# Kernel tuning notes

Hardware: AMD Instinct MI355X
Metric: run time of the kernel (lower is better)

The kernel has to match this reference:

```python
import jax, jax.numpy as jnp
import numpy as np

DIM = 768

def setup_inputs() -> dict:
    key = jax.random.key(0)
    k1, k2, k3, k4, k5 = jax.random.split(key, 5)
    B, S, D = 16, 1024, DIM
    x = jax.random.normal(k1, (B, S, D), dtype=jnp.float32)
    # torch Linear weights: W has shape [out, in], y = x @ W.T + b
    w_qkv = jax.random.normal(k2, (3 * D, D), dtype=jnp.float32) * (D ** -0.5)
    b_qkv = jax.random.normal(k3, (3 * D,), dtype=jnp.float32) * 0.01
    w_out = jax.random.normal(k4, (D, D), dtype=jnp.float32) * (D ** -0.5)
    b_out = jax.random.normal(k5, (D,), dtype=jnp.float32) * 0.01
    return {"x": x, "w_qkv": w_qkv, "b_qkv": b_qkv, "w_out": w_out, "b_out": b_out}

def reference(x, w_qkv, b_qkv, w_out, b_out):
    D = x.shape[-1]
    qkv = jnp.einsum('bsd,ed->bse', x, w_qkv) + b_qkv  # [B,S,3D]
    q, k, v = jnp.split(qkv, 3, axis=-1)
    scale = D ** -0.5
    att = jnp.einsum('bqd,bkd->bqk', q, k) * scale  # [B,S,S]
    att = jax.nn.softmax(att, axis=-1)
    # dropout (p=0.1) is identity in eval mode
    out = jnp.einsum('bqk,bkd->bqd', att, v)
    return jnp.einsum('bsd,ed->bse', out, w_out) + b_out
```

## Files before the change

kernel.cpp:

```cpp
#include <hip/hip_runtime.h>
#include <hip/hip_bf16.h>
#include <math.h>

typedef __attribute__((ext_vector_type(8))) short bf16x8;
typedef __attribute__((ext_vector_type(4))) float f32x4;

__device__ __forceinline__ unsigned short f2bf_rne(float f) {
    union { float f; unsigned u; } x; x.f = f;
    unsigned r = x.u + 0x7FFFu + ((x.u >> 16) & 1u);
    return (unsigned short)(r >> 16);
}
__device__ __forceinline__ float bf2f(unsigned short u) {
    union { unsigned u; float f; } x; x.u = ((unsigned)u) << 16; return x.f;
}

__device__ __forceinline__ void store4(unsigned short* p, float v0, float v1, float v2, float v3) {
    ushort4 o; o.x = f2bf_rne(v0); o.y = f2bf_rne(v1); o.z = f2bf_rne(v2); o.w = f2bf_rne(v3);
    *(ushort4*)p = o;
}
__device__ __forceinline__ void store4(float* p, float v0, float v1, float v2, float v3) {
    float4 o; o.x = v0; o.y = v1; o.z = v2; o.w = v3;
    *(float4*)p = o;
}

__device__ __forceinline__ void async_copy16(const void* g, void* l) {
    __builtin_amdgcn_global_load_lds(
        (const __attribute__((address_space(1))) void*)g,
        (__attribute__((address_space(3))) void*)l, 16, 0, 0);
}

__global__ __launch_bounds__(256) void cvt_all(
    const float* __restrict__ x, const float* __restrict__ wo,
    unsigned short* __restrict__ xb, unsigned short* __restrict__ wob,
    float4* __restrict__ z1, float4* __restrict__ z2,
    int n4x, int n4o, int n4r, int n4z)
{
    int j = blockIdx.x * 256 + threadIdx.x;
    const float* in; unsigned short* out;
    if (j < n4x) { in = x; out = xb; }
    else {
        j -= n4x;
        if (j < n4o) { in = wo; out = wob; }
        else {
            j -= n4o;
            if (j < n4r) { float4 z = {0.f, 0.f, 0.f, 0.f}; z1[j] = z; return; }
            j -= n4r;
            if (j < n4z) { float4 z = {0.f, 0.f, 0.f, 0.f}; z2[j] = z; }
            return;
        }
    }
    float4 v = ((const float4*)in)[j];
    ushort4 o;
    o.x = f2bf_rne(v.x); o.y = f2bf_rne(v.y);
    o.z = f2bf_rne(v.z); o.w = f2bf_rne(v.w);
    ((ushort4*)out)[j] = o;
}

__global__ __launch_bounds__(256) void prep(
    const float* __restrict__ w_qkv, const float* __restrict__ b_qkv,
    const float* __restrict__ w_out, const float* __restrict__ b_out,
    unsigned short* __restrict__ wqT, unsigned short* __restrict__ wkT,
    unsigned short* __restrict__ wvT,
    float* __restrict__ v1f, float* __restrict__ v2f,
    float* __restrict__ bpp, float* __restrict__ cbuf)
{
    const int blk = blockIdx.x;
    const int t   = threadIdx.x;
    if (blk < 432) {
        __shared__ float sh[64][65];
        __shared__ float pv[4][64];
        const int m  = blk / 144;
        const int r  = blk % 144;
        const int ty = r / 12;
        const int tx = r % 12;
        const float* W = w_qkv + (long long)m * 768 * 768;
        unsigned short* WT = (m == 0) ? wqT : (m == 1) ? wkT : wvT;
        const float* bsrc = (m == 0) ? (b_qkv + 768) : b_qkv;
        const int il = t & 63;
        const int ob = t >> 6;
        float acc = 0.f;
#pragma unroll
        for (int it = 0; it < 16; ++it) {
            const int ol = ob + it * 4;
            float w = W[(long long)(ty * 64 + ol) * 768 + tx * 64 + il];
            sh[ol][il] = w;
            if (m < 2) acc += w * bsrc[ty * 64 + ol];
        }
        __syncthreads();
#pragma unroll
        for (int it = 0; it < 16; ++it) {
            const int il2 = ob + it * 4;
            WT[(long long)(tx * 64 + il2) * 768 + ty * 64 + il] = f2bf_rne(sh[il][il2]);
        }
        if (m < 2) {
            pv[ob][il] = acc;
            __syncthreads();
            if (t < 64) {
                float s = pv[0][t] + pv[1][t] + pv[2][t] + pv[3][t];
                atomicAdd((m == 0 ? v1f : v2f) + tx * 64 + t, s);
            }
        }
    } else if (blk < 624) {
        const int d = (blk - 432) * 4 + (t >> 6);
        const int l = t & 63;
        float s = 0.f;
        for (int o = l; o < 768; o += 64)
            s += w_out[(long long)d * 768 + o] * b_qkv[1536 + o];
        for (int off = 1; off < 64; off <<= 1) s += __shfl_xor(s, off);
        if (l == 0) bpp[d] = b_out[d] + s;
    } else {
        if (t < 64) {
            float s = 0.f;
            for (int o = t; o < 768; o += 64) s += b_qkv[o] * b_qkv[768 + o];
            for (int off = 1; off < 64; off <<= 1) s += __shfl_xor(s, off);
            if (t == 0) cbuf[0] = s;
        }
    }
}

__global__ __launch_bounds__(256) void finishprep(
    const float* __restrict__ v1f, const float* __restrict__ v2f,
    unsigned short* __restrict__ B2)
{
    int i = blockIdx.x * 256 + threadIdx.x;
    if (i < 768) {
        B2[1536LL * 768 + i] = f2bf_rne(v1f[i]);
        B2[1537LL * 768 + i] = f2bf_rne(v2f[i]);
    }
}

template <typename OutT, bool DO_EXP, bool DO_RSCALE, bool DO_VT>
__global__ __launch_bounds__(256) void gemm_nt_bf16(
    const unsigned short* __restrict__ A, int lda, long long strideA,
    const unsigned short* __restrict__ B, int ldb, long long strideB,
    OutT* __restrict__ C, int ldc, long long strideC,
    const float* __restrict__ bias, float scale, int K,
    float* __restrict__ rowsum, const float* __restrict__ rscale,
    unsigned short* __restrict__ vtp)
{
    __shared__ unsigned short shA[128 * 64];
    __shared__ unsigned short shB[128 * 64];

    const int t    = threadIdx.x;
    const int lane = t & 63;
    const int wave = t >> 6;
    const int wm   = (wave & 1) * 64;
    const int wn   = (wave >> 1) * 64;
    const int quad = lane >> 4;
    const int l16  = lane & 15;

    const int gx = gridDim.x, gy = gridDim.y;
    const int nwg = gx * gy * gridDim.z;
    const int orig = blockIdx.x + gx * (blockIdx.y + gy * blockIdx.z);
    const int id  = (orig & 7) * (nwg >> 3) + (orig >> 3);
    const int bx  = id % gx;
    const int rem = id / gx;
    const int by  = rem % gy;
    const int bz  = rem / gy;

    const long long batch = bz;
    A += batch * strideA;
    B += batch * strideB;
    C += batch * strideC;

    const long long tileM = (long long)by * 128;
    const long long tileN = (long long)bx * 128;
    const long long rowsPerBatch = (long long)gy * 128;

    f32x4 acc[4][4];
#pragma unroll
    for (int i = 0; i < 4; ++i)
#pragma unroll
        for (int j = 0; j < 4; ++j)
#pragma unroll
            for (int r = 0; r < 4; ++r) acc[i][j][r] = 0.0f;

    for (int k0 = 0; k0 < K; k0 += 64) {
        __syncthreads();
#pragma unroll
        for (int p = 0; p < 4; ++p) {
            const int g   = p * 256 + t;
            const int row = g >> 3;
            const int kg  = (g & 7) ^ (row & 7);
            async_copy16(A + (tileM + row) * (long long)lda + k0 + kg * 8, &shA[g << 3]);
            async_copy16(B + (tileN + row) * (long long)ldb + k0 + kg * 8, &shB[g << 3]);
        }
        __syncthreads();

#pragma unroll 1
        for (int h = 0; h < 2; ++h) {
            bf16x8 af[4], bfr[4];
#pragma unroll
            for (int mi = 0; mi < 4; ++mi) {
                const int row = wm + mi * 16 + l16;
                const int kg  = ((h << 2) | quad) ^ (row & 7);
                af[mi] = *(const bf16x8*)(&shA[row * 64 + kg * 8]);
            }
#pragma unroll
            for (int ni = 0; ni < 4; ++ni) {
                const int row = wn + ni * 16 + l16;
                const int kg  = ((h << 2) | quad) ^ (row & 7);
                bfr[ni] = *(const bf16x8*)(&shB[row * 64 + kg * 8]);
            }
#pragma unroll
            for (int mi = 0; mi < 4; ++mi)
#pragma unroll
                for (int ni = 0; ni < 4; ++ni)
                    acc[mi][ni] = __builtin_amdgcn_mfma_f32_16x16x32_bf16(
                        bfr[ni], af[mi], acc[mi][ni], 0, 0, 0);
        }
    }

    const bool vt_block = DO_VT && (tileN >= 768) && (tileN < 1536);
    float cadd = 0.f;
    if (DO_EXP) cadd = rscale[0];
#pragma unroll
    for (int mi = 0; mi < 4; ++mi) {
        const long long gm = tileM + wm + mi * 16 + l16;
        float w = scale;
        if (DO_RSCALE) w = scale / rscale[batch * rowsPerBatch + gm];
        float uq = 0.f;
        if (DO_EXP) uq = bf2f(A[gm * (long long)lda + K + 768]) + cadd;
        float rsum = 0.0f;
#pragma unroll
        for (int ni = 0; ni < 4; ++ni) {
            const long long gn0 = tileN + wn + ni * 16 + quad * 4;
            float b0 = 0.f, b1 = 0.f, b2 = 0.f, b3 = 0.f;
            if (bias) {
                float4 bv = *(const float4*)&bias[gn0];
                b0 = bv.x; b1 = bv.y; b2 = bv.z; b3 = bv.w;
            }
            const f32x4 a = acc[mi][ni];
            float v0, v1, v2, v3;
            if (DO_EXP) {
                const float w0 = bf2f(A[(gn0 + 0) * (long long)lda + K + 769]);
                const float w1 = bf2f(A[(gn0 + 1) * (long long)lda + K + 769]);
                const float w2 = bf2f(A[(gn0 + 2) * (long long)lda + K + 769]);
                const float w3 = bf2f(A[(gn0 + 3) * (long long)lda + K + 769]);
                v0 = __expf((a[0] + uq + w0) * scale);
                v1 = __expf((a[1] + uq + w1) * scale);
                v2 = __expf((a[2] + uq + w2) * scale);
                v3 = __expf((a[3] + uq + w3) * scale);
                rsum += (v0 + v1) + (v2 + v3);
            } else {
                v0 = a[0] * w + b0; v1 = a[1] * w + b1;
                v2 = a[2] * w + b2; v3 = a[3] * w + b3;
            }
            if (vt_block) {
                const long long b_i  = gm >> 10;
                const long long kin  = gm & 1023;
                unsigned short* vp = vtp + (b_i * 768 + (gn0 - 768)) * 1024 + kin;
                vp[0]        = f2bf_rne(v0);
                vp[1024]     = f2bf_rne(v1);
                vp[2 * 1024] = f2bf_rne(v2);
                vp[3 * 1024] = f2bf_rne(v3);
            } else {
                store4(C + gm * (long long)ldc + gn0, v0, v1, v2, v3);
            }
        }
        if (DO_EXP) {
            rsum += __shfl_xor(rsum, 16);
            rsum += __shfl_xor(rsum, 32);
            if (quad == 0)
                atomicAdd(&rowsum[batch * rowsPerBatch + gm], rsum);
        }
    }
}

extern "C" void kernel_launch(void* const* d_in, const int* in_sizes, int n_in,
                              void* d_out, int out_size, void* d_ws, size_t ws_size,
                              hipStream_t stream) {
    (void)in_sizes; (void)n_in; (void)out_size; (void)ws_size;

    const float* x     = (const float*)d_in[0];
    const float* w_qkv = (const float*)d_in[1];
    const float* b_qkv = (const float*)d_in[2];
    const float* w_out = (const float*)d_in[3];
    const float* b_out = (const float*)d_in[4];
    float* out = (float*)d_out;

    const int B = 16, S = 1024, D = 768;
    const long long MS = (long long)B * S;
    const int NB2 = 1664;

    unsigned short* xb  = (unsigned short*)d_ws;
    unsigned short* wob = xb  + MS * D;
    unsigned short* wqT = wob + (long long)D * D;
    unsigned short* wkT = wqT + (long long)D * D;
    unsigned short* wvT = wkT + (long long)D * D;
    unsigned short* B2  = wvT + (long long)D * D;
    unsigned short* xm  = B2  + (long long)NB2 * D;
    unsigned short* vwt = xm  + MS * NB2;
    unsigned short* att = vwt + (long long)B * D * S;
    float* rsum = (float*)(att + (long long)B * S * S);
    float* v1f  = rsum + MS;
    float* v2f  = v1f + D;
    float* bpp  = v2f + D;
    float* cbuf = bpp + D;

    {
        const int n4x = (int)(MS * D / 4);
        const int n4o = D * D / 4;
        const int n4r = (int)((MS + 2 * D) / 4);
        const int n4z = (NB2 - 1538) * D * 2 / 16;
        const int tot = n4x + n4o + n4r + n4z;
        cvt_all<<<(tot + 255) / 256, 256, 0, stream>>>(
            x, w_out, xb, wob, (float4*)rsum, (float4*)(B2 + 1538LL * D),
            n4x, n4o, n4r, n4z);
    }

    prep<<<625, 256, 0, stream>>>(w_qkv, b_qkv, w_out, b_out,
                                  wqT, wkT, wvT, v1f, v2f, bpp, cbuf);

    finishprep<<<3, 256, 0, stream>>>(v1f, v2f, B2);

    gemm_nt_bf16<unsigned short, false, false, false><<<dim3(6, 6, 2), 256, 0, stream>>>(
        wkT, D, (long long)(wob - wkT),
        wqT, D, (long long)(wvT - wqT),
        B2,  D, (long long)D * D,
        nullptr, 1.0f, D, nullptr, nullptr, nullptr);

    gemm_nt_bf16<unsigned short, false, false, true><<<dim3(NB2 / 128, (int)(MS / 128), 1), 256, 0, stream>>>(
        xb, D, 0, B2, D, 0, xm, NB2, 0, nullptr, 1.0f, D, nullptr, nullptr, vwt);

    const float scale = 0.03608439182435162f;
    gemm_nt_bf16<unsigned short, true, false, false><<<dim3(S / 128, S / 128, B), 256, 0, stream>>>(
        xm, NB2, (long long)S * NB2,
        xb, D,   (long long)S * D,
        att, S,  (long long)S * S, nullptr, scale, D, rsum, cbuf, nullptr);

    gemm_nt_bf16<float, false, true, false><<<dim3(D / 128, S / 128, B), 256, 0, stream>>>(
        att, S, (long long)S * S,
        vwt, S, (long long)D * S,
        out, D, (long long)S * D, bpp, 1.0f, S, nullptr, rsum, nullptr);
}
```

Baseline: 279.1 us.

## Compute bias-dot terms in fp32 x-conversion, stage V^T stores through LDS

The extra bias-projection columns are removed from the big projection GEMM (N from 1664 to 1536). The per-row u and w dot products are now computed in fp32 inside a new x-conversion kernel, and the attention epilogue reads them from small float arrays instead of doing strided bf16 reads from xm. The transposed V write is staged through shared memory so each thread writes contiguous 8-byte chunks instead of scattered 2-byte stores. Atomics in prep are replaced by partial sums plus a small reduce kernel, and the w_out conversion and rowsum zeroing move into prep. This adds kernel launches and an extra LDS barrier in the projection GEMM.

```diff
diff --git a/kernel.cpp b/kernel.cpp
--- a/kernel.cpp
+++ b/kernel.cpp
@@ -10,9 +10,6 @@
     unsigned r = x.u + 0x7FFFu + ((x.u >> 16) & 1u);
     return (unsigned short)(r >> 16);
 }
-__device__ __forceinline__ float bf2f(unsigned short u) {
-    union { unsigned u; float f; } x; x.u = ((unsigned)u) << 16; return x.f;
-}
 
 __device__ __forceinline__ void store4(unsigned short* p, float v0, float v1, float v2, float v3) {
     ushort4 o; o.x = f2bf_rne(v0); o.y = f2bf_rne(v1); o.z = f2bf_rne(v2); o.w = f2bf_rne(v3);
@@ -29,40 +26,13 @@
         (__attribute__((address_space(3))) void*)l, 16, 0, 0);
 }
 
-__global__ __launch_bounds__(256) void cvt_all(
-    const float* __restrict__ x, const float* __restrict__ wo,
-    unsigned short* __restrict__ xb, unsigned short* __restrict__ wob,
-    float4* __restrict__ z1, float4* __restrict__ z2,
-    int n4x, int n4o, int n4r, int n4z)
-{
-    int j = blockIdx.x * 256 + threadIdx.x;
-    const float* in; unsigned short* out;
-    if (j < n4x) { in = x; out = xb; }
-    else {
-        j -= n4x;
-        if (j < n4o) { in = wo; out = wob; }
-        else {
-            j -= n4o;
-            if (j < n4r) { float4 z = {0.f, 0.f, 0.f, 0.f}; z1[j] = z; return; }
-            j -= n4r;
-            if (j < n4z) { float4 z = {0.f, 0.f, 0.f, 0.f}; z2[j] = z; }
-            return;
-        }
-    }
-    float4 v = ((const float4*)in)[j];
-    ushort4 o;
-    o.x = f2bf_rne(v.x); o.y = f2bf_rne(v.y);
-    o.z = f2bf_rne(v.z); o.w = f2bf_rne(v.w);
-    ((ushort4*)out)[j] = o;
-}
-
 __global__ __launch_bounds__(256) void prep(
     const float* __restrict__ w_qkv, const float* __restrict__ b_qkv,
     const float* __restrict__ w_out, const float* __restrict__ b_out,
     unsigned short* __restrict__ wqT, unsigned short* __restrict__ wkT,
-    unsigned short* __restrict__ wvT,
-    float* __restrict__ v1f, float* __restrict__ v2f,
-    float* __restrict__ bpp, float* __restrict__ cbuf)
+    unsigned short* __restrict__ wvT, unsigned short* __restrict__ wob,
+    float* __restrict__ vpart, float* __restrict__ bpp, float* __restrict__ cbuf,
+    float* __restrict__ rsum)
 {
     const int blk = blockIdx.x;
     const int t   = threadIdx.x;
@@ -97,7 +67,7 @@
             __syncthreads();
             if (t < 64) {
                 float s = pv[0][t] + pv[1][t] + pv[2][t] + pv[3][t];
-                atomicAdd((m == 0 ? v1f : v2f) + tx * 64 + t, s);
+                vpart[(m * 12 + ty) * 768 + tx * 64 + t] = s;
             }
         }
     } else if (blk < 624) {
@@ -108,25 +78,70 @@
             s += w_out[(long long)d * 768 + o] * b_qkv[1536 + o];
         for (int off = 1; off < 64; off <<= 1) s += __shfl_xor(s, off);
         if (l == 0) bpp[d] = b_out[d] + s;
-    } else {
+    } else if (blk == 624) {
         if (t < 64) {
             float s = 0.f;
             for (int o = t; o < 768; o += 64) s += b_qkv[o] * b_qkv[768 + o];
             for (int off = 1; off < 64; off <<= 1) s += __shfl_xor(s, off);
             if (t == 0) cbuf[0] = s;
         }
-    }
-}
-
-__global__ __launch_bounds__(256) void finishprep(
+    } else if (blk < 1201) {
+        const int j = (blk - 625) * 256 + t;
+        float4 v = ((const float4*)w_out)[j];
+        ushort4 o;
+        o.x = f2bf_rne(v.x); o.y = f2bf_rne(v.y);
+        o.z = f2bf_rne(v.z); o.w = f2bf_rne(v.w);
+        ((ushort4*)wob)[j] = o;
+    } else {
+        const int j = (blk - 1201) * 256 + t;
+        float4 z = {0.f, 0.f, 0.f, 0.f};
+        ((float4*)rsum)[j] = z;
+    }
+}
+
+__global__ __launch_bounds__(256) void finishv(
+    const float* __restrict__ vpart, float* __restrict__ v1f, float* __restrict__ v2f)
+{
+    const int j = blockIdx.x * 256 + threadIdx.x;
+    const int m = (j >= 768);
+    const int i = j - m * 768;
+    float s = 0.f;
+#pragma unroll
+    for (int ty = 0; ty < 12; ++ty) s += vpart[(m * 12 + ty) * 768 + i];
+    (m ? v2f : v1f)[i] = s;
+}
+
+__global__ __launch_bounds__(256) void cvt_x(
+    const float* __restrict__ x, unsigned short* __restrict__ xb,
     const float* __restrict__ v1f, const float* __restrict__ v2f,
-    unsigned short* __restrict__ B2)
+    float* __restrict__ uf, float* __restrict__ wf)
 {
-    int i = blockIdx.x * 256 + threadIdx.x;
-    if (i < 768) {
-        B2[1536LL * 768 + i] = f2bf_rne(v1f[i]);
-        B2[1537LL * 768 + i] = f2bf_rne(v2f[i]);
-    }
+    const int wave = threadIdx.x >> 6;
+    const int lane = threadIdx.x & 63;
+    const long long row = (long long)blockIdx.x * 4 + wave;
+    const float4* xr = (const float4*)x + row * 192;
+    ushort4* xbr = (ushort4*)xb + row * 192;
+    const float4* v1 = (const float4*)v1f;
+    const float4* v2 = (const float4*)v2f;
+    float u = 0.f, w = 0.f;
+#pragma unroll
+    for (int j = 0; j < 3; ++j) {
+        const int c = j * 64 + lane;
+        float4 v = xr[c];
+        ushort4 o;
+        o.x = f2bf_rne(v.x); o.y = f2bf_rne(v.y);
+        o.z = f2bf_rne(v.z); o.w = f2bf_rne(v.w);
+        xbr[c] = o;
+        float4 a = v1[c], b = v2[c];
+        u += v.x * a.x + v.y * a.y + v.z * a.z + v.w * a.w;
+        w += v.x * b.x + v.y * b.y + v.z * b.z + v.w * b.w;
+    }
+#pragma unroll
+    for (int off = 1; off < 64; off <<= 1) {
+        u += __shfl_xor(u, off);
+        w += __shfl_xor(w, off);
+    }
+    if (lane == 0) { uf[row] = u; wf[row] = w; }
 }
 
 template <typename OutT, bool DO_EXP, bool DO_RSCALE, bool DO_VT>
@@ -136,10 +151,11 @@
     OutT* __restrict__ C, int ldc, long long strideC,
     const float* __restrict__ bias, float scale, int K,
     float* __restrict__ rowsum, const float* __restrict__ rscale,
-    unsigned short* __restrict__ vtp)
+    unsigned short* __restrict__ vtp,
+    const float* __restrict__ uf, const float* __restrict__ wf)
 {
-    __shared__ unsigned short shA[128 * 64];
-    __shared__ unsigned short shB[128 * 64];
+    __shared__ unsigned short shA[8448];
+    __shared__ unsigned short shB[8448];
 
     const int t    = threadIdx.x;
     const int lane = t & 63;
@@ -212,15 +228,19 @@
     }
 
     const bool vt_block = DO_VT && (tileN >= 768) && (tileN < 1536);
+    if (vt_block) __syncthreads();
+    unsigned short* const shd = (wn == 0) ? shA : shB;
     float cadd = 0.f;
     if (DO_EXP) cadd = rscale[0];
+    const float* ufb = DO_EXP ? (uf + batch * rowsPerBatch) : nullptr;
+    const float* wfb = DO_EXP ? (wf + batch * rowsPerBatch) : nullptr;
 #pragma unroll
     for (int mi = 0; mi < 4; ++mi) {
         const long long gm = tileM + wm + mi * 16 + l16;
         float w = scale;
         if (DO_RSCALE) w = scale / rscale[batch * rowsPerBatch + gm];
         float uq = 0.f;
-        if (DO_EXP) uq = bf2f(A[gm * (long long)lda + K + 768]) + cadd;
+        if (DO_EXP) uq = ufb[gm] + cadd;
         float rsum = 0.0f;
 #pragma unroll
         for (int ni = 0; ni < 4; ++ni) {
@@ -233,10 +253,10 @@
             const f32x4 a = acc[mi][ni];
             float v0, v1, v2, v3;
             if (DO_EXP) {
-                const float w0 = bf2f(A[(gn0 + 0) * (long long)lda + K + 769]);
-                const float w1 = bf2f(A[(gn0 + 1) * (long long)lda + K + 769]);
-                const float w2 = bf2f(A[(gn0 + 2) * (long long)lda + K + 769]);
-                const float w3 = bf2f(A[(gn0 + 3) * (long long)lda + K + 769]);
+                const float w0 = wfb[gn0 + 0];
+                const float w1 = wfb[gn0 + 1];
+                const float w2 = wfb[gn0 + 2];
+                const float w3 = wfb[gn0 + 3];
                 v0 = __expf((a[0] + uq + w0) * scale);
                 v1 = __expf((a[1] + uq + w1) * scale);
                 v2 = __expf((a[2] + uq + w2) * scale);
@@ -247,13 +267,12 @@
                 v2 = a[2] * w + b2; v3 = a[3] * w + b3;
             }
             if (vt_block) {
-                const long long b_i  = gm >> 10;
-                const long long kin  = gm & 1023;
-                unsigned short* vp = vtp + (b_i * 768 + (gn0 - 768)) * 1024 + kin;
-                vp[0]        = f2bf_rne(v0);
-                vp[1024]     = f2bf_rne(v1);
-                vp[2 * 1024] = f2bf_rne(v2);
-                vp[3 * 1024] = f2bf_rne(v3);
+                const int dl = ni * 16 + quad * 4;
+                const int kl = wm + mi * 16 + l16;
+                shd[(dl + 0) * 132 + kl] = f2bf_rne(v0);
+                shd[(dl + 1) * 132 + kl] = f2bf_rne(v1);
+                shd[(dl + 2) * 132 + kl] = f2bf_rne(v2);
+                shd[(dl + 3) * 132 + kl] = f2bf_rne(v3);
             } else {
                 store4(C + gm * (long long)ldc + gn0, v0, v1, v2, v3);
             }
@@ -264,6 +283,19 @@
             if (quad == 0)
                 atomicAdd(&rowsum[batch * rowsPerBatch + gm], rsum);
         }
+    }
+    if (vt_block) {
+        __syncthreads();
+        const long long bvt  = tileM >> 10;
+        const long long kin0 = tileM & 1023;
+        const int dr = t >> 1;
+        const int hf = t & 1;
+        const unsigned short* src = (dr < 64) ? &shA[dr * 132] : &shB[(dr - 64) * 132];
+        unsigned short* dst = vtp + (bvt * 768 + (tileN - 768) + dr) * 1024 + kin0 + hf * 64;
+        src += hf * 64;
+#pragma unroll
+        for (int j = 0; j < 16; ++j)
+            *(uint2*)(dst + j * 4) = *(const uint2*)(src + j * 4);
     }
 }
 
@@ -281,7 +313,7 @@
 
     const int B = 16, S = 1024, D = 768;
     const long long MS = (long long)B * S;
-    const int NB2 = 1664;
+    const int NB2 = 1536;
 
     unsigned short* xb  = (unsigned short*)d_ws;
     unsigned short* wob = xb  + MS * D;
@@ -292,45 +324,39 @@
     unsigned short* xm  = B2  + (long long)NB2 * D;
     unsigned short* vwt = xm  + MS * NB2;
     unsigned short* att = vwt + (long long)B * D * S;
-    float* rsum = (float*)(att + (long long)B * S * S);
-    float* v1f  = rsum + MS;
-    float* v2f  = v1f + D;
-    float* bpp  = v2f + D;
-    float* cbuf = bpp + D;
-
-    {
-        const int n4x = (int)(MS * D / 4);
-        const int n4o = D * D / 4;
-        const int n4r = (int)((MS + 2 * D) / 4);
-        const int n4z = (NB2 - 1538) * D * 2 / 16;
-        const int tot = n4x + n4o + n4r + n4z;
-        cvt_all<<<(tot + 255) / 256, 256, 0, stream>>>(
-            x, w_out, xb, wob, (float4*)rsum, (float4*)(B2 + 1538LL * D),
-            n4x, n4o, n4r, n4z);
-    }
-
-    prep<<<625, 256, 0, stream>>>(w_qkv, b_qkv, w_out, b_out,
-                                  wqT, wkT, wvT, v1f, v2f, bpp, cbuf);
-
-    finishprep<<<3, 256, 0, stream>>>(v1f, v2f, B2);
+    float* rsum  = (float*)(att + (long long)B * S * S);
+    float* v1f   = rsum + MS;
+    float* v2f   = v1f + D;
+    float* bpp   = v2f + D;
+    float* cbuf  = bpp + D;
+    float* uf    = cbuf + 4;
+    float* wf    = uf + MS;
+    float* vpart = wf + MS;
+
+    prep<<<1217, 256, 0, stream>>>(w_qkv, b_qkv, w_out, b_out,
+                                   wqT, wkT, wvT, wob, vpart, bpp, cbuf, rsum);
+
+    finishv<<<6, 256, 0, stream>>>(vpart, v1f, v2f);
 
     gemm_nt_bf16<unsigned short, false, false, false><<<dim3(6, 6, 2), 256, 0, stream>>>(
         wkT, D, (long long)(wob - wkT),
         wqT, D, (long long)(wvT - wqT),
         B2,  D, (long long)D * D,
-        nullptr, 1.0f, D, nullptr, nullptr, nullptr);
+        nullptr, 1.0f, D, nullptr, nullptr, nullptr, nullptr, nullptr);
+
+    cvt_x<<<4096, 256, 0, stream>>>(x, xb, v1f, v2f, uf, wf);
 
     gemm_nt_bf16<unsigned short, false, false, true><<<dim3(NB2 / 128, (int)(MS / 128), 1), 256, 0, stream>>>(
-        xb, D, 0, B2, D, 0, xm, NB2, 0, nullptr, 1.0f, D, nullptr, nullptr, vwt);
+        xb, D, 0, B2, D, 0, xm, NB2, 0, nullptr, 1.0f, D, nullptr, nullptr, vwt, nullptr, nullptr);
 
     const float scale = 0.03608439182435162f;
     gemm_nt_bf16<unsigned short, true, false, false><<<dim3(S / 128, S / 128, B), 256, 0, stream>>>(
         xm, NB2, (long long)S * NB2,
         xb, D,   (long long)S * D,
-        att, S,  (long long)S * S, nullptr, scale, D, rsum, cbuf, nullptr);
+        att, S,  (long long)S * S, nullptr, scale, D, rsum, cbuf, nullptr, uf, wf);
 
     gemm_nt_bf16<float, false, true, false><<<dim3(D / 128, S / 128, B), 256, 0, stream>>>(
         att, S, (long long)S * S,
         vwt, S, (long long)D * S,
-        out, D, (long long)S * D, bpp, 1.0f, S, nullptr, rsum, nullptr);
-}
+        out, D, (long long)S * D, bpp, 1.0f, S, nullptr, rsum, nullptr, nullptr, nullptr);
+}
```

New measurement: 274.1 us. Within noise of the previous version (-1.8%).
